# Kernel optimization log

Measured on AMD Instinct MI355X. Metric: run time of the kernel, lower is better.

## Reference

```python
import jax, jax.numpy as jnp
import numpy as np

D_MODEL, N_HEADS, D_HEAD = 1024, 16, 64
BATCH, SEQ = 4, 2048


def setup_inputs() -> dict:
    key = jax.random.key(0)
    ks = jax.random.split(key, 10)
    s = 1.0 / np.sqrt(D_MODEL)
    x = jax.random.normal(ks[0], (BATCH, SEQ, D_MODEL), dtype=jnp.float32)
    attention_mask = jax.random.randint(ks[1], (BATCH, SEQ), 0, 2).astype(jnp.bool_)
    # guarantee at least one attended key per batch row (avoid all -inf softmax)
    attention_mask = attention_mask.at[:, 0].set(True)
    def lin(k):
        kw, kb = jax.random.split(k)
        W = jax.random.uniform(kw, (D_MODEL, D_MODEL), jnp.float32, -s, s)
        b = jax.random.uniform(kb, (D_MODEL,), jnp.float32, -s, s)
        return W, b
    Wq, bq = lin(ks[2]); Wk, bk = lin(ks[3]); Wv, bv = lin(ks[4]); Wo, bo = lin(ks[5])
    return {"x": x, "attention_mask": attention_mask,
            "Wq": Wq, "bq": bq, "Wk": Wk, "bk": bk,
            "Wv": Wv, "bv": bv, "Wo": Wo, "bo": bo}


def reference(x, attention_mask, Wq, bq, Wk, bk, Wv, bv, Wo, bo):
    B, S, _ = x.shape
    def proj(W, b):  # [B,S,d_model] -> [B,S,H,Dh]
        return (x @ W + b).reshape(B, S, N_HEADS, D_HEAD)
    q = proj(Wq, bq)
    k = proj(Wk, bk)
    v = proj(Wv, bv)
    scores = jnp.einsum('bqhd,bkhd->bhqk', q, k)  # [B,H,S,S]
    add_mask = jnp.where(attention_mask, 0.0, jnp.inf)[:, None, None, :]
    # faithful order: subtract mask, THEN scale (inf survives division)
    probs = jax.nn.softmax((scores - add_mask) / jnp.sqrt(jnp.float32(D_HEAD)), axis=-1)
    attn = jnp.einsum('bhqk,bkhd->bqhd', probs, v).reshape(B, S, N_HEADS * D_HEAD)
    return attn @ Wo + bo
```

## Files before the change

kernel.cpp:

```cpp
#include <hip/hip_runtime.h>
#include <hip/hip_bf16.h>
#include <math.h>

#define BATCH 4
#define SEQ   2048
#define DM    1024
#define NH    16
#define DH    64
#define MROWS (BATCH * SEQ)

typedef unsigned short ushort_t;
typedef unsigned int   uint_t;
typedef __attribute__((ext_vector_type(8))) short  short8;
typedef __attribute__((ext_vector_type(4))) float  float4v;

#define QSCALE 0.1803368801111244f

__device__ __forceinline__ ushort_t f2bf(float v) {
    uint_t u = __float_as_uint(v);
    u += 0x7FFFu + ((u >> 16) & 1u);
    return (ushort_t)(u >> 16);
}
__device__ __forceinline__ float bf2f(ushort_t h) {
    return __uint_as_float(((uint_t)h) << 16);
}
__device__ __forceinline__ void gload_lds16(const ushort_t* g, ushort_t* lds) {
    __builtin_amdgcn_global_load_lds(
        (const __attribute__((address_space(1))) void*)g,
        (__attribute__((address_space(3))) void*)lds, 16, 0, 0);
}

__global__ __launch_bounds__(256) void conv_x(
    const float* __restrict__ src, ushort_t* __restrict__ dst, int n4)
{
    int i = blockIdx.x * 256 + threadIdx.x;
    if (i >= n4) return;
    float4 v = ((const float4*)src)[i];
    ((ushort4*)dst)[i] = make_ushort4(f2bf(v.x), f2bf(v.y), f2bf(v.z), f2bf(v.w));
}

__global__ __launch_bounds__(256) void convT_w4(
    const float* __restrict__ W0, const float* __restrict__ W1,
    const float* __restrict__ W2, const float* __restrict__ W3,
    ushort_t* __restrict__ fused, ushort_t* __restrict__ woh,
    ushort_t* __restrict__ wol)
{
    __shared__ float sT[64][65];
    const int z = blockIdx.z;
    const float* W = (z == 0) ? W0 : (z == 1) ? W1 : (z == 2) ? W2 : W3;
    ushort_t* ht = (z < 3) ? fused + (size_t)z * 1024 * 1024 : woh;
    const int n0 = blockIdx.x * 64, k0 = blockIdx.y * 64;
    const int t = threadIdx.x;
#pragma unroll
    for (int i = 0; i < 16; i++) {
        int idx = t + i * 256, r = idx >> 6, c = idx & 63;
        sT[r][c] = W[(size_t)(k0 + r) * 1024 + n0 + c];
    }
    __syncthreads();
#pragma unroll
    for (int i = 0; i < 16; i++) {
        int idx = t + i * 256, r = idx >> 6, c = idx & 63;
        float v = sT[c][r];
        ushort_t h = f2bf(v);
        ht[(size_t)(n0 + r) * 1024 + k0 + c] = h;
        if (z == 3) wol[(size_t)(n0 + r) * 1024 + k0 + c] = f2bf(v - bf2f(h));
    }
}

#define BAR()   asm volatile("s_barrier" ::: "memory")
#define LGKM0() asm volatile("s_waitcnt lgkmcnt(0)" ::: "memory")
#define VMW6()  asm volatile("s_waitcnt vmcnt(6)" ::: "memory")

#define STAGE_A(BO, KT) do {                                                 \
    const ushort_t* _s = prowA + (size_t)((KT) & 15) * 64;                   \
    gload_lds16(_s,         &smem[(BO) + dstw]);                             \
    gload_lds16(_s + 65536, &smem[(BO) + 4096 + dstw]);                      \
  } while (0)

#define STAGE_B(BO, KT) do {                                                 \
    const ushort_t* _s = prowB + (size_t)((KT) & 15) * 64;                   \
    gload_lds16(_s,          &smem[(BO) + 8192  + dstw]);                    \
    gload_lds16(_s + 65536,  &smem[(BO) + 12288 + dstw]);                    \
    gload_lds16(_s + 131072, &smem[(BO) + 16384 + dstw]);                    \
    gload_lds16(_s + 196608, &smem[(BO) + 20480 + dstw]);                    \
  } while (0)

#define LOAD_AV(BO) do {                                                     \
    _Pragma("unroll")                                                        \
    for (int mf = 0; mf < 4; mf++) {                                         \
      av[mf][0] = *(const short8*)&smem[(BO) + aAm + mf * 1024 + aA0];       \
      av[mf][1] = *(const short8*)&smem[(BO) + aAm + mf * 1024 + aA1];       \
    }                                                                        \
  } while (0)

#define LOAD_BV(BO, NQ) do {                                                 \
    _Pragma("unroll")                                                        \
    for (int nf = 0; nf < 2; nf++) {                                         \
      bvf[nf][0] = *(const short8*)&smem[(BO) + 8192 + aBn + (NQ) * 2048 +   \
                                         nf * 1024 + aA0];                   \
      bvf[nf][1] = *(const short8*)&smem[(BO) + 8192 + aBn + (NQ) * 2048 +   \
                                         nf * 1024 + aA1];                   \
    }                                                                        \
  } while (0)

#define MFMA_H(NQ) do {                                                      \
    __builtin_amdgcn_s_setprio(1);                                           \
    _Pragma("unroll")                                                        \
    for (int kk = 0; kk < 2; kk++)                                           \
      _Pragma("unroll")                                                      \
      for (int nf = 0; nf < 2; nf++)                                         \
        _Pragma("unroll")                                                    \
        for (int mf = 0; mf < 4; mf++)                                       \
          acc[mf][(NQ) * 2 + nf] =                                           \
              __builtin_amdgcn_mfma_f32_16x16x32_bf16(                       \
                  av[mf][kk], bvf[nf][kk], acc[mf][(NQ) * 2 + nf], 0, 0, 0); \
    __builtin_amdgcn_s_setprio(0);                                           \
  } while (0)

__global__ __launch_bounds__(512, 2) void gemm_qkv(
    const ushort_t* __restrict__ A, const ushort_t* __restrict__ Bt,
    const float* __restrict__ bq, const float* __restrict__ bk,
    const float* __restrict__ bv, const int* __restrict__ mask,
    ushort_t* __restrict__ Qh, ushort_t* __restrict__ Kh,
    ushort_t* __restrict__ Vt)
{
    __shared__ __align__(16) ushort_t smem[73728];
    const int t = threadIdx.x, lane = t & 63, w = t >> 6;

    int bid = blockIdx.y * 12 + blockIdx.x;
    bid = (bid & 7) * 96 + (bid >> 3);
    const int n0 = (bid % 12) * 256, m0 = (bid / 12) * 128;

    const int wm = w >> 2, wn = w & 3;
    const int lq = lane >> 4, lc = lane & 15;
    const int gl = (lane & 7) ^ ((lane >> 3) & 7);
    const int sect = n0 >> 10;
    const float* bsel = (sect == 0) ? bq : (sect == 1) ? bk : bv;
    const float scl = (sect == 0) ? QSCALE : 1.0f;

    const ushort_t* prowA = A  + (size_t)(m0 + w * 8 + (lane >> 3)) * 1024 + gl * 8;
    const ushort_t* prowB = Bt + (size_t)(n0 + w * 8 + (lane >> 3)) * 1024 + gl * 8;
    const int dstw = w * 512;

    const int aA0 = lc * 64 + ((lq ^ (lc & 7)) * 8);
    const int aA1 = lc * 64 + (((4 + lq) ^ (lc & 7)) * 8);
    const int aAm = wm * 4096;
    const int aBn = wn * 4096;

    float4v acc[4][4];
#pragma unroll
    for (int i = 0; i < 4; i++)
#pragma unroll
        for (int j = 0; j < 4; j++) acc[i][j] = (float4v)(0.0f);

    short8 av[4][2], bvf[2][2];

    STAGE_A(0, 0); STAGE_B(0, 0); STAGE_A(24576, 1); STAGE_B(24576, 1);
    VMW6();
    BAR();

    int bc = 0, bs = 49152;
    for (int kt = 0; kt < 16; kt++) {
        LOAD_AV(bc); LOAD_BV(bc, 0); STAGE_A(bs, kt + 2);
        BAR(); LGKM0(); MFMA_H(0); BAR();
        LOAD_BV(bc, 1); STAGE_B(bs, kt + 2);
        BAR(); LGKM0(); MFMA_H(1); VMW6(); BAR();
        bc = (bc == 49152) ? 0 : bc + 24576;
        bs = (bs == 49152) ? 0 : bs + 24576;
    }

#pragma unroll
    for (int nf = 0; nf < 4; nf++) {
        const int nn = (n0 + wn * 64 + nf * 16 + lc) & 1023;
        const float bvv = bsel[nn];
        const int h = nn >> 6, d = nn & 63;
#pragma unroll
        for (int mf = 0; mf < 4; mf++) {
            const int mbase = m0 + wm * 64 + mf * 16 + lq * 4;
            const int b = mbase >> 11, s0 = mbase & 2047;
            int mk[4] = {1, 1, 1, 1};
            if (sect != 0) {
                const int4 m4 = *(const int4*)&mask[b * 2048 + s0];
                mk[0] = m4.x; mk[1] = m4.y; mk[2] = m4.z; mk[3] = m4.w;
            }
            if (sect == 2) {
                ushort_t hh[4];
#pragma unroll
                for (int r = 0; r < 4; r++)
                    hh[r] = mk[r] ? f2bf(acc[mf][nf][r] + bvv) : (ushort_t)0;
                *(ushort4*)&Vt[((size_t)(b * 16 + h) * 64 + d) * 2048 + s0] =
                    make_ushort4(hh[0], hh[1], hh[2], hh[3]);
            } else {
                ushort_t* dst = (sect == 0) ? Qh : Kh;
#pragma unroll
                for (int r = 0; r < 4; r++)
                    dst[((size_t)(b * 16 + h) * 2048 + s0 + r) * 64 + d] =
                        mk[r] ? f2bf((acc[mf][nf][r] + bvv) * scl) : (ushort_t)0;
            }
        }
    }
}

#undef STAGE_A
#undef STAGE_B
#undef LOAD_AV
#undef LOAD_BV
#undef MFMA_H

#define S3_STAGE3A(BO, KT) do {                                              \
    const size_t _k = (size_t)((KT) & 31) * 32;                              \
    gload_lds16(pAh + _k, &smem[(BO) + toff]);                               \
    gload_lds16(pAl + _k, &smem[(BO) + 4096 + toff]);                        \
    gload_lds16(pBh + _k, &smem[(BO) + 8192 + toff]);                        \
  } while (0)

#define S3_STAGE3B(BO, KT) do {                                              \
    const size_t _k = (size_t)((KT) & 31) * 32;                              \
    gload_lds16(pBh + 131072 + _k, &smem[(BO) + 12288 + toff]);              \
    gload_lds16(pBl + _k,          &smem[(BO) + 16384 + toff]);              \
    gload_lds16(pBl + 131072 + _k, &smem[(BO) + 20480 + toff]);              \
  } while (0)

#define S3_MFMA(NQ) do {                                                     \
    __builtin_amdgcn_s_setprio(1);                                           \
    _Pragma("unroll")                                                        \
    for (int nf = 0; nf < 2; nf++)                                           \
      _Pragma("unroll")                                                      \
      for (int mf = 0; mf < 4; mf++) {                                       \
        float4v* _a = &acc[mf][(NQ) * 2 + nf];                               \
        *_a = __builtin_amdgcn_mfma_f32_16x16x32_bf16(ah[mf], bh[nf], *_a, 0, 0, 0); \
        *_a = __builtin_amdgcn_mfma_f32_16x16x32_bf16(al[mf], bh[nf], *_a, 0, 0, 0); \
        *_a = __builtin_amdgcn_mfma_f32_16x16x32_bf16(ah[mf], bl[nf], *_a, 0, 0, 0); \
      }                                                                      \
    __builtin_amdgcn_s_setprio(0);                                           \
  } while (0)

__global__ __launch_bounds__(512, 2) void gemm_split3(
    const ushort_t* __restrict__ Ah, const ushort_t* __restrict__ Al,
    const ushort_t* __restrict__ Bh, const ushort_t* __restrict__ Bl,
    const float* __restrict__ bias, float* __restrict__ out)
{
    __shared__ __align__(16) ushort_t smem[73728];
    const int t = threadIdx.x, lane = t & 63, w = t >> 6;

    int bid = blockIdx.y * 4 + blockIdx.x;
    bid = (bid & 7) * 32 + (bid >> 3);
    const int n0 = (bid % 4) * 256, m0 = (bid / 4) * 128;

    const int wm = w >> 2, wn = w & 3;
    const int lq = lane >> 4, lc = lane & 15;

    const int prow = t >> 2;
    const int pc = (t & 3) ^ (prow & 3);
    const size_t offA = (size_t)(m0 + prow) * 1024 + pc * 8;
    const size_t offB = (size_t)(n0 + prow) * 1024 + pc * 8;
    const ushort_t* pAh = Ah + offA;
    const ushort_t* pAl = Al + offA;
    const ushort_t* pBh = Bh + offB;
    const ushort_t* pBl = Bl + offB;
    const int toff = t * 8;

    const int aR = lc * 32 + ((lq ^ (lc & 3)) * 8);
    const int aAm = wm * 2048;
    const int aBn = wn * 2048;

    float4v acc[4][4];
#pragma unroll
    for (int i = 0; i < 4; i++)
#pragma unroll
        for (int j = 0; j < 4; j++) acc[i][j] = (float4v)(0.0f);

    short8 ah[4], al[4], bh[2], bl[2];

    S3_STAGE3A(0, 0);     S3_STAGE3B(0, 0);
    S3_STAGE3A(24576, 1); S3_STAGE3B(24576, 1);
    VMW6();
    BAR();

    int bc = 0, bs = 49152;
    for (int kt = 0; kt < 32; kt++) {
#pragma unroll
        for (int mf = 0; mf < 4; mf++) {
            ah[mf] = *(const short8*)&smem[bc + aAm + mf * 512 + aR];
            al[mf] = *(const short8*)&smem[bc + 4096 + aAm + mf * 512 + aR];
        }
#pragma unroll
        for (int nf = 0; nf < 2; nf++) {
            bh[nf] = *(const short8*)&smem[bc + 8192 + aBn + nf * 512 + aR];
            bl[nf] = *(const short8*)&smem[bc + 16384 + aBn + nf * 512 + aR];
        }
        S3_STAGE3A(bs, kt + 2);
        BAR(); LGKM0(); S3_MFMA(0); BAR();

#pragma unroll
        for (int nf = 0; nf < 2; nf++) {
            bh[nf] = *(const short8*)&smem[bc + 8192 + aBn + 1024 + nf * 512 + aR];
            bl[nf] = *(const short8*)&smem[bc + 16384 + aBn + 1024 + nf * 512 + aR];
        }
        S3_STAGE3B(bs, kt + 2);
        BAR(); LGKM0(); S3_MFMA(1); VMW6(); BAR();

        bc = (bc == 49152) ? 0 : bc + 24576;
        bs = (bs == 49152) ? 0 : bs + 24576;
    }

#pragma unroll
    for (int nf = 0; nf < 4; nf++) {
        const int n = n0 + wn * 64 + nf * 16 + lc;
        const float bvv = bias[n];
#pragma unroll
        for (int mf = 0; mf < 4; mf++)
#pragma unroll
            for (int r = 0; r < 4; r++) {
                const int m = m0 + wm * 64 + mf * 16 + lq * 4 + r;
                out[(size_t)m * 1024 + n] = acc[mf][nf][r] + bvv;
            }
    }
}

#undef S3_STAGE3A
#undef S3_STAGE3B
#undef S3_MFMA
#undef BAR
#undef LGKM0
#undef VMW6

__global__ __launch_bounds__(512, 4) void flash_mfma(
    const ushort_t* __restrict__ Q, const ushort_t* __restrict__ K,
    const ushort_t* __restrict__ Vt, const int* __restrict__ mask,
    ushort_t* __restrict__ Oh, ushort_t* __restrict__ Ol)
{
    __shared__ __align__(16) ushort_t smem[32768];
    const int t = threadIdx.x, lane = t & 63, w = t >> 6;
    const int q0 = blockIdx.x * 256;
    const int bh = blockIdx.y, b = bh >> 4, h = bh & 15;
    const int lq = lane >> 4, lc = lane & 15;
    const int wm = w * 32;
    const int gl = (lane & 7) ^ ((lane >> 3) & 7);
    const int lc7 = lc & 7;

    const short8 onesf = (short8)(lc == 0 ? (short)0x3F80 : (short)0);

    {
        const int4 a = ((const int4*)(mask + b * SEQ))[t];
        int cnt = (a.x == 0) + (a.y == 0) + (a.z == 0) + (a.w == 0);
#pragma unroll
        for (int off = 1; off < 64; off <<= 1) cnt += __shfl_xor(cnt, off);
        if (lane == 0) ((float*)&smem[28672])[w] = (float)cnt;
    }
#pragma unroll
    for (int j = 0; j < 4; j++) {
        const int i = w * 4 + j;
        gload_lds16(Q + ((size_t)bh * SEQ + q0 + i * 8 + (lane >> 3)) * 64 + gl * 8,
                    &smem[i * 512]);
    }
    const ushort_t* gsrc;
    int gstride, jstride, dstb;
    if (w < 4) {
        gsrc = K + ((size_t)bh * SEQ + w * 16 + (lane >> 3)) * 64 + gl * 8;
        gstride = 64 * 64;  jstride = 8 * 64;   dstb = 16384 + w * 1024;
    } else {
        gsrc = Vt + ((size_t)bh * 64 + (w - 4) * 16 + (lane >> 3)) * SEQ + gl * 8;
        gstride = 64;       jstride = 8 * SEQ;  dstb = 24576 + (w - 4) * 1024;
    }
    gload_lds16(gsrc,           &smem[dstb]);
    gload_lds16(gsrc + jstride, &smem[dstb + 512]);
    gsrc += gstride;

    __syncthreads();

    const float* cs = (const float*)&smem[28672];
    const float nmaskf = cs[0] + cs[1] + cs[2] + cs[3] +
                         cs[4] + cs[5] + cs[6] + cs[7];

    short8 aq[2][2];
#pragma unroll
    for (int mt = 0; mt < 2; mt++)
#pragma unroll
        for (int kk = 0; kk < 2; kk++) {
            const int r = wm + mt * 16 + lc;
            aq[mt][kk] = *(const short8*)&smem[r * 64 + (((kk * 4 + lq) ^ (r & 7)) * 8)];
        }

    int aK[2], aPw[4], aPr[2];
#pragma unroll
    for (int kk = 0; kk < 2; kk++) {
        aK[kk]  = lc * 64 + (((kk * 4 + lq) ^ lc7) * 8);
        aPr[kk] = wm * 64 + aK[kk];
    }
#pragma unroll
    for (int kt4 = 0; kt4 < 4; kt4++)
        aPw[kt4] = wm * 64 + lc * 64 + (((kt4 * 2 + (lq >> 1)) ^ lc7) * 8) + (lq & 1) * 4;

    float4v O[2][4];
    float4v lacc[2];
#pragma unroll
    for (int mt = 0; mt < 2; mt++) {
#pragma unroll
        for (int nt = 0; nt < 4; nt++) O[mt][nt] = (float4v)(0.0f);
        lacc[mt] = (float4v)(0.0f);
    }

    __syncthreads();

    for (int kt = 0; kt < 32; kt++) {
        const int cur = (kt & 1) * 4096;
        const int nxt = cur ^ 4096;

        if (kt < 31) {
            gload_lds16(gsrc,           &smem[dstb + nxt]);
            gload_lds16(gsrc + jstride, &smem[dstb + nxt + 512]);
            gsrc += gstride;
        }

#pragma unroll
        for (int kt4 = 0; kt4 < 4; kt4++) {
            float4v s0 = (float4v)(0.0f), s1 = (float4v)(0.0f);
#pragma unroll
            for (int kk = 0; kk < 2; kk++) {
                short8 ak = *(const short8*)&smem[16384 + cur + kt4 * 1024 + aK[kk]];
                s0 = __builtin_amdgcn_mfma_f32_16x16x32_bf16(ak, aq[0][kk], s0, 0, 0, 0);
                s1 = __builtin_amdgcn_mfma_f32_16x16x32_bf16(ak, aq[1][kk], s1, 0, 0, 0);
            }
            {
                const float p0 = __builtin_amdgcn_exp2f(s0[0]);
                const float p1 = __builtin_amdgcn_exp2f(s0[1]);
                const float p2 = __builtin_amdgcn_exp2f(s0[2]);
                const float p3 = __builtin_amdgcn_exp2f(s0[3]);
                __hip_bfloat162 pk01 = __float22bfloat162_rn(make_float2(p0, p1));
                __hip_bfloat162 pk23 = __float22bfloat162_rn(make_float2(p2, p3));
                *(uint2*)&smem[aPw[kt4]] =
                    make_uint2(*(const uint_t*)&pk01, *(const uint_t*)&pk23);
            }
            {
                const float p0 = __builtin_amdgcn_exp2f(s1[0]);
                const float p1 = __builtin_amdgcn_exp2f(s1[1]);
                const float p2 = __builtin_amdgcn_exp2f(s1[2]);
                const float p3 = __builtin_amdgcn_exp2f(s1[3]);
                __hip_bfloat162 pk01 = __float22bfloat162_rn(make_float2(p0, p1));
                __hip_bfloat162 pk23 = __float22bfloat162_rn(make_float2(p2, p3));
                *(uint2*)&smem[1024 + aPw[kt4]] =
                    make_uint2(*(const uint_t*)&pk01, *(const uint_t*)&pk23);
            }
        }

#pragma unroll
        for (int kk = 0; kk < 2; kk++) {
            short8 ap[2];
#pragma unroll
            for (int mt = 0; mt < 2; mt++)
                ap[mt] = *(const short8*)&smem[mt * 1024 + aPr[kk]];
            __builtin_amdgcn_s_setprio(1);
#pragma unroll
            for (int mt = 0; mt < 2; mt++)
                lacc[mt] = __builtin_amdgcn_mfma_f32_16x16x32_bf16(ap[mt], onesf, lacc[mt], 0, 0, 0);
#pragma unroll
            for (int nt = 0; nt < 4; nt++) {
                short8 bv = *(const short8*)&smem[24576 + cur + nt * 1024 + aK[kk]];
#pragma unroll
                for (int mt = 0; mt < 2; mt++)
                    O[mt][nt] = __builtin_amdgcn_mfma_f32_16x16x32_bf16(ap[mt], bv, O[mt][nt], 0, 0, 0);
            }
            __builtin_amdgcn_s_setprio(0);
        }

        asm volatile("s_waitcnt vmcnt(0)" ::: "memory");
        asm volatile("s_barrier" ::: "memory");
    }

#pragma unroll
    for (int mt = 0; mt < 2; mt++) {
#pragma unroll
        for (int r = 0; r < 4; r++) {
            const float lsum = __shfl(lacc[mt][r], lane & 48) - nmaskf;
            const float inv = 1.0f / lsum;
            const int srow = q0 + wm + mt * 16 + lq * 4 + r;
#pragma unroll
            for (int nt = 0; nt < 4; nt++) {
                const float v = O[mt][nt][r] * inv;
                const ushort_t hh = f2bf(v);
                const size_t idx = ((size_t)(b * SEQ + srow)) * 1024 + h * 64 + nt * 16 + lc;
                Oh[idx] = hh;
                Ol[idx] = f2bf(v - bf2f(hh));
            }
        }
    }
}

extern "C" void kernel_launch(void* const* d_in, const int* in_sizes, int n_in,
                              void* d_out, int out_size, void* d_ws, size_t ws_size,
                              hipStream_t stream) {
    const float* x    = (const float*)d_in[0];
    const int*   mask = (const int*)d_in[1];
    const float* Wq   = (const float*)d_in[2];
    const float* bq   = (const float*)d_in[3];
    const float* Wk   = (const float*)d_in[4];
    const float* bk   = (const float*)d_in[5];
    const float* Wv   = (const float*)d_in[6];
    const float* bv   = (const float*)d_in[7];
    const float* Wo   = (const float*)d_in[8];
    const float* bo   = (const float*)d_in[9];
    float* out = (float*)d_out;

    ushort_t* p = (ushort_t*)d_ws;
    const size_t PLANE  = (size_t)MROWS * DM;
    const size_t WPLANE = (size_t)DM * DM;
    ushort_t* xh  = p;  p += PLANE;
    ushort_t* wf  = p;  p += 3 * WPLANE;
    ushort_t* woh = p;  p += WPLANE;
    ushort_t* wol = p;  p += WPLANE;
    ushort_t* Qh  = p;  p += PLANE;
    ushort_t* Kh  = p;  p += PLANE;
    ushort_t* Vth = p;  p += PLANE;
    ushort_t* Ath = p;  p += PLANE;
    ushort_t* Atl = p;  p += PLANE;

    dim3 blk(256);
    hipLaunchKernelGGL(conv_x, dim3(8192), blk, 0, stream, x, xh, 2097152);
    hipLaunchKernelGGL(convT_w4, dim3(16, 16, 4), blk, 0, stream,
                       Wq, Wk, Wv, Wo, wf, woh, wol);
    hipLaunchKernelGGL(gemm_qkv, dim3(12, 64), dim3(512), 0, stream,
                       xh, wf, bq, bk, bv, mask, Qh, Kh, Vth);
    hipLaunchKernelGGL(flash_mfma, dim3(8, 64), dim3(512), 0, stream,
                       Qh, Kh, Vth, mask, Ath, Atl);
    hipLaunchKernelGGL(gemm_split3, dim3(4, 64), dim3(512), 0, stream,
                       Ath, Atl, woh, wol, bo, out);
}
```

Baseline: 311.4 us.

## Enlarge flash attention query tile, triple-buffer K/V, and grid-stride x conversion

The flash attention kernel now processes 512 queries per block (64 rows per wave) instead of 256. K/V tiles are shared by more MFMAs, and K/V loads go through a three-stage LDS ring with a partial vmcnt wait instead of a full drain each iteration. The row-sum is accumulated in VALU from the rounded bf16 probabilities rather than by an extra MFMA against a ones vector. The block index is remapped so neighbouring blocks share heads. The x conversion kernel becomes a 4-iteration grid-stride loop with a quarter of the blocks. Larger tiles raise register and LDS use: occupancy drops to 2 blocks per CU and the grid shrinks to 256 blocks.

```diff
diff --git a/kernel.cpp b/kernel.cpp
--- a/kernel.cpp
+++ b/kernel.cpp
@@ -34,9 +34,11 @@
     const float* __restrict__ src, ushort_t* __restrict__ dst, int n4)
 {
     int i = blockIdx.x * 256 + threadIdx.x;
-    if (i >= n4) return;
-    float4 v = ((const float4*)src)[i];
-    ((ushort4*)dst)[i] = make_ushort4(f2bf(v.x), f2bf(v.y), f2bf(v.z), f2bf(v.w));
+#pragma unroll
+    for (int k = 0; k < 4; k++, i += 524288) {
+        float4 v = ((const float4*)src)[i];
+        ((ushort4*)dst)[i] = make_ushort4(f2bf(v.x), f2bf(v.y), f2bf(v.z), f2bf(v.w));
+    }
 }
 
 __global__ __launch_bounds__(256) void convT_w4(
@@ -325,156 +327,168 @@
 #undef LGKM0
 #undef VMW6
 
-__global__ __launch_bounds__(512, 4) void flash_mfma(
+#define FBAR()  asm volatile("s_barrier" ::: "memory")
+#define FVMW4() asm volatile("s_waitcnt vmcnt(4)" ::: "memory")
+
+__global__ __launch_bounds__(512, 2) void flash_mfma(
     const ushort_t* __restrict__ Q, const ushort_t* __restrict__ K,
     const ushort_t* __restrict__ Vt, const int* __restrict__ mask,
     ushort_t* __restrict__ Oh, ushort_t* __restrict__ Ol)
 {
-    __shared__ __align__(16) ushort_t smem[32768];
+    __shared__ __align__(16) ushort_t smem[57344];
     const int t = threadIdx.x, lane = t & 63, w = t >> 6;
-    const int q0 = blockIdx.x * 256;
-    const int bh = blockIdx.y, b = bh >> 4, h = bh & 15;
-    const int lq = lane >> 4, lc = lane & 15;
-    const int wm = w * 32;
-    const int gl = (lane & 7) ^ ((lane >> 3) & 7);
-    const int lc7 = lc & 7;
-
-    const short8 onesf = (short8)(lc == 0 ? (short)0x3F80 : (short)0);
-
-    {
-        const int4 a = ((const int4*)(mask + b * SEQ))[t];
-        int cnt = (a.x == 0) + (a.y == 0) + (a.z == 0) + (a.w == 0);
-#pragma unroll
-        for (int off = 1; off < 64; off <<= 1) cnt += __shfl_xor(cnt, off);
-        if (lane == 0) ((float*)&smem[28672])[w] = (float)cnt;
-    }
-#pragma unroll
-    for (int j = 0; j < 4; j++) {
-        const int i = w * 4 + j;
-        gload_lds16(Q + ((size_t)bh * SEQ + q0 + i * 8 + (lane >> 3)) * 64 + gl * 8,
-                    &smem[i * 512]);
-    }
-    const ushort_t* gsrc;
-    int gstride, jstride, dstb;
-    if (w < 4) {
-        gsrc = K + ((size_t)bh * SEQ + w * 16 + (lane >> 3)) * 64 + gl * 8;
-        gstride = 64 * 64;  jstride = 8 * 64;   dstb = 16384 + w * 1024;
-    } else {
-        gsrc = Vt + ((size_t)bh * 64 + (w - 4) * 16 + (lane >> 3)) * SEQ + gl * 8;
-        gstride = 64;       jstride = 8 * SEQ;  dstb = 24576 + (w - 4) * 1024;
-    }
-    gload_lds16(gsrc,           &smem[dstb]);
-    gload_lds16(gsrc + jstride, &smem[dstb + 512]);
-    gsrc += gstride;
-
-    __syncthreads();
-
-    const float* cs = (const float*)&smem[28672];
+
+    const int i = blockIdx.y * 4 + blockIdx.x;
+    const int bh = (i & 7) + ((i >> 5) << 3);
+    const int q0 = ((i >> 3) & 3) * 512;
+    const int b = bh >> 4, h = bh & 15;
+
+    const int lq = lane >> 4, lc = lane & 15, lc7 = lc & 7;
+    const int wq = w * 64;
+
+    const int4 ma = ((const int4*)(mask + b * SEQ))[t];
+
+    const int trow = lane >> 3;
+    const int gl = (lane & 7) ^ (trow & 7);
+    const ushort_t* qsrc = Q + ((size_t)bh * SEQ + q0 + wq + trow) * 64 + gl * 8;
+#pragma unroll
+    for (int j = 0; j < 8; j++)
+        gload_lds16(qsrc + j * 512, &smem[w * 4096 + j * 512 + lane * 8]);
+
+    const int strow = t >> 3;
+    const int sgl = (t & 7) ^ (strow & 7);
+    const ushort_t* kbase = K  + ((size_t)bh * SEQ + strow) * 64 + sgl * 8;
+    const ushort_t* vbase = Vt + ((size_t)bh * 64 + strow) * SEQ + sgl * 8;
+    gload_lds16(kbase,        &smem[32768 + t * 8]);
+    gload_lds16(vbase,        &smem[45056 + t * 8]);
+    gload_lds16(kbase + 4096, &smem[32768 + 4096 + t * 8]);
+    gload_lds16(vbase + 64,   &smem[45056 + 4096 + t * 8]);
+
+    int cnt = (ma.x == 0) + (ma.y == 0) + (ma.z == 0) + (ma.w == 0);
+#pragma unroll
+    for (int off = 1; off < 64; off <<= 1) cnt += __shfl_xor(cnt, off);
+    if (lane == 0) ((float*)&smem[40960])[w] = (float)cnt;
+
+    FBAR();
+
+    const float* cs = (const float*)&smem[40960];
     const float nmaskf = cs[0] + cs[1] + cs[2] + cs[3] +
                          cs[4] + cs[5] + cs[6] + cs[7];
 
-    short8 aq[2][2];
-#pragma unroll
-    for (int mt = 0; mt < 2; mt++)
+    FVMW4();
+    short8 aq[4][2];
+#pragma unroll
+    for (int mt = 0; mt < 4; mt++)
 #pragma unroll
         for (int kk = 0; kk < 2; kk++) {
-            const int r = wm + mt * 16 + lc;
-            aq[mt][kk] = *(const short8*)&smem[r * 64 + (((kk * 4 + lq) ^ (r & 7)) * 8)];
-        }
-
-    int aK[2], aPw[4], aPr[2];
-#pragma unroll
-    for (int kk = 0; kk < 2; kk++) {
-        aK[kk]  = lc * 64 + (((kk * 4 + lq) ^ lc7) * 8);
-        aPr[kk] = wm * 64 + aK[kk];
-    }
+            const int r = mt * 16 + lc;
+            aq[mt][kk] = *(const short8*)&smem[w * 4096 + r * 64 +
+                                               (((kk * 4 + lq) ^ (r & 7)) * 8)];
+        }
+    FBAR();
+
+    int aK[2], aPw[4];
+#pragma unroll
+    for (int kk = 0; kk < 2; kk++)
+        aK[kk] = lc * 64 + (((kk * 4 + lq) ^ lc7) * 8);
 #pragma unroll
     for (int kt4 = 0; kt4 < 4; kt4++)
-        aPw[kt4] = wm * 64 + lc * 64 + (((kt4 * 2 + (lq >> 1)) ^ lc7) * 8) + (lq & 1) * 4;
-
-    float4v O[2][4];
-    float4v lacc[2];
-#pragma unroll
-    for (int mt = 0; mt < 2; mt++) {
+        aPw[kt4] = lc * 64 + (((kt4 * 2 + (lq >> 1)) ^ lc7) * 8) + (lq & 1) * 4;
+
+    float4v O[4][4];
+    float ladd[4];
+#pragma unroll
+    for (int mt = 0; mt < 4; mt++) {
 #pragma unroll
         for (int nt = 0; nt < 4; nt++) O[mt][nt] = (float4v)(0.0f);
-        lacc[mt] = (float4v)(0.0f);
-    }
-
-    __syncthreads();
-
+        ladd[mt] = 0.0f;
+    }
+
+    int cb = 0, sb = 2;
     for (int kt = 0; kt < 32; kt++) {
-        const int cur = (kt & 1) * 4096;
-        const int nxt = cur ^ 4096;
-
-        if (kt < 31) {
-            gload_lds16(gsrc,           &smem[dstb + nxt]);
-            gload_lds16(gsrc + jstride, &smem[dstb + nxt + 512]);
-            gsrc += gstride;
-        }
+        const int kn = (kt + 2) & 31;
+        gload_lds16(kbase + kn * 4096, &smem[32768 + sb * 4096 + t * 8]);
+        gload_lds16(vbase + kn * 64,   &smem[45056 + sb * 4096 + t * 8]);
+        FVMW4();
+        FBAR();
+
+        const int kb = 32768 + cb * 4096;
+        const int vb = 45056 + cb * 4096;
+        const int pb = w * 4096;
 
 #pragma unroll
         for (int kt4 = 0; kt4 < 4; kt4++) {
-            float4v s0 = (float4v)(0.0f), s1 = (float4v)(0.0f);
+            float4v sc[4];
+#pragma unroll
+            for (int mt = 0; mt < 4; mt++) sc[mt] = (float4v)(0.0f);
 #pragma unroll
             for (int kk = 0; kk < 2; kk++) {
-                short8 ak = *(const short8*)&smem[16384 + cur + kt4 * 1024 + aK[kk]];
-                s0 = __builtin_amdgcn_mfma_f32_16x16x32_bf16(ak, aq[0][kk], s0, 0, 0, 0);
-                s1 = __builtin_amdgcn_mfma_f32_16x16x32_bf16(ak, aq[1][kk], s1, 0, 0, 0);
-            }
-            {
-                const float p0 = __builtin_amdgcn_exp2f(s0[0]);
-                const float p1 = __builtin_amdgcn_exp2f(s0[1]);
-                const float p2 = __builtin_amdgcn_exp2f(s0[2]);
-                const float p3 = __builtin_amdgcn_exp2f(s0[3]);
+                const short8 ak = *(const short8*)&smem[kb + kt4 * 1024 + aK[kk]];
+#pragma unroll
+                for (int mt = 0; mt < 4; mt++)
+                    sc[mt] = __builtin_amdgcn_mfma_f32_16x16x32_bf16(ak, aq[mt][kk], sc[mt], 0, 0, 0);
+            }
+#pragma unroll
+            for (int mt = 0; mt < 4; mt++) {
+                const float p0 = __builtin_amdgcn_exp2f(sc[mt][0]);
+                const float p1 = __builtin_amdgcn_exp2f(sc[mt][1]);
+                const float p2 = __builtin_amdgcn_exp2f(sc[mt][2]);
+                const float p3 = __builtin_amdgcn_exp2f(sc[mt][3]);
                 __hip_bfloat162 pk01 = __float22bfloat162_rn(make_float2(p0, p1));
                 __hip_bfloat162 pk23 = __float22bfloat162_rn(make_float2(p2, p3));
-                *(uint2*)&smem[aPw[kt4]] =
-                    make_uint2(*(const uint_t*)&pk01, *(const uint_t*)&pk23);
-            }
-            {
-                const float p0 = __builtin_amdgcn_exp2f(s1[0]);
-                const float p1 = __builtin_amdgcn_exp2f(s1[1]);
-                const float p2 = __builtin_amdgcn_exp2f(s1[2]);
-                const float p3 = __builtin_amdgcn_exp2f(s1[3]);
-                __hip_bfloat162 pk01 = __float22bfloat162_rn(make_float2(p0, p1));
-                __hip_bfloat162 pk23 = __float22bfloat162_rn(make_float2(p2, p3));
-                *(uint2*)&smem[1024 + aPw[kt4]] =
-                    make_uint2(*(const uint_t*)&pk01, *(const uint_t*)&pk23);
+                const uint_t u01 = *(const uint_t*)&pk01;
+                const uint_t u23 = *(const uint_t*)&pk23;
+                ladd[mt] += __uint_as_float(u01 << 16) + __uint_as_float(u01 & 0xffff0000u)
+                          + __uint_as_float(u23 << 16) + __uint_as_float(u23 & 0xffff0000u);
+                *(uint2*)&smem[pb + mt * 1024 + aPw[kt4]] = make_uint2(u01, u23);
             }
         }
 
 #pragma unroll
         for (int kk = 0; kk < 2; kk++) {
-            short8 ap[2];
-#pragma unroll
-            for (int mt = 0; mt < 2; mt++)
-                ap[mt] = *(const short8*)&smem[mt * 1024 + aPr[kk]];
+            short8 ap[4];
+#pragma unroll
+            for (int mt = 0; mt < 4; mt++)
+                ap[mt] = *(const short8*)&smem[pb + mt * 1024 + aK[kk]];
             __builtin_amdgcn_s_setprio(1);
 #pragma unroll
-            for (int mt = 0; mt < 2; mt++)
-                lacc[mt] = __builtin_amdgcn_mfma_f32_16x16x32_bf16(ap[mt], onesf, lacc[mt], 0, 0, 0);
-#pragma unroll
             for (int nt = 0; nt < 4; nt++) {
-                short8 bv = *(const short8*)&smem[24576 + cur + nt * 1024 + aK[kk]];
-#pragma unroll
-                for (int mt = 0; mt < 2; mt++)
+                const short8 bv = *(const short8*)&smem[vb + nt * 1024 + aK[kk]];
+#pragma unroll
+                for (int mt = 0; mt < 4; mt++)
                     O[mt][nt] = __builtin_amdgcn_mfma_f32_16x16x32_bf16(ap[mt], bv, O[mt][nt], 0, 0, 0);
             }
             __builtin_amdgcn_s_setprio(0);
         }
-
-        asm volatile("s_waitcnt vmcnt(0)" ::: "memory");
-        asm volatile("s_barrier" ::: "memory");
-    }
-
-#pragma unroll
-    for (int mt = 0; mt < 2; mt++) {
+        FBAR();
+
+        cb = (cb == 2) ? 0 : cb + 1;
+        sb = (sb == 2) ? 0 : sb + 1;
+    }
+
+    float lred[4];
+#pragma unroll
+    for (int mt = 0; mt < 4; mt++) {
+        float v = ladd[mt];
+        v += __shfl_xor(v, 16);
+        v += __shfl_xor(v, 32);
+        lred[mt] = v;
+    }
+    if (lq == 0) {
+#pragma unroll
+        for (int mt = 0; mt < 4; mt++)
+            ((float*)smem)[w * 2048 + mt * 16 + lc] = lred[mt];
+    }
+    __syncthreads();
+
+#pragma unroll
+    for (int mt = 0; mt < 4; mt++) {
 #pragma unroll
         for (int r = 0; r < 4; r++) {
-            const float lsum = __shfl(lacc[mt][r], lane & 48) - nmaskf;
+            const float lsum =
+                ((const float*)smem)[w * 2048 + mt * 16 + lq * 4 + r] - nmaskf;
             const float inv = 1.0f / lsum;
-            const int srow = q0 + wm + mt * 16 + lq * 4 + r;
+            const int srow = q0 + wq + mt * 16 + lq * 4 + r;
 #pragma unroll
             for (int nt = 0; nt < 4; nt++) {
                 const float v = O[mt][nt][r] * inv;
@@ -486,6 +500,9 @@
         }
     }
 }
+
+#undef FBAR
+#undef FVMW4
 
 extern "C" void kernel_launch(void* const* d_in, const int* in_sizes, int n_in,
                               void* d_out, int out_size, void* d_ws, size_t ws_size,
@@ -516,12 +533,12 @@
     ushort_t* Atl = p;  p += PLANE;
 
     dim3 blk(256);
-    hipLaunchKernelGGL(conv_x, dim3(8192), blk, 0, stream, x, xh, 2097152);
+    hipLaunchKernelGGL(conv_x, dim3(2048), blk, 0, stream, x, xh, 2097152);
     hipLaunchKernelGGL(convT_w4, dim3(16, 16, 4), blk, 0, stream,
                        Wq, Wk, Wv, Wo, wf, woh, wol);
     hipLaunchKernelGGL(gemm_qkv, dim3(12, 64), dim3(512), 0, stream,
                        xh, wf, bq, bk, bv, mask, Qh, Kh, Vth);
-    hipLaunchKernelGGL(flash_mfma, dim3(8, 64), dim3(512), 0, stream,
+    hipLaunchKernelGGL(flash_mfma, dim3(4, 64), dim3(512), 0, stream,
                        Qh, Kh, Vth, mask, Ath, Atl);
     hipLaunchKernelGGL(gemm_split3, dim3(4, 64), dim3(512), 0, stream,
                        Ath, Atl, woh, wol, bo, out);
```

Result: slower. 323.8 us (+4.0%).

## Merge conversion kernels into one launch and remap flash attention block order

Applied to the files above, without the earlier changes.

Combines the x bf16 conversion and the weight transpose/convert kernels into a single prep launch: the first 2048 blocks each convert four float4s per thread, and the remaining 1024 blocks transpose the weights. This removes one kernel launch and its inter-kernel gap. It also remaps the flash attention grid so that consecutive blocks cover different batch-head pairs and the query tile varies slowest, which changes how work is spread across CUs and how K/V is reused in cache. The remap risks worse L2 locality if K/V sharing between query tiles of the same head was helping.

```diff
diff --git a/kernel.cpp b/kernel.cpp
--- a/kernel.cpp
+++ b/kernel.cpp
@@ -30,27 +30,31 @@
         (__attribute__((address_space(3))) void*)lds, 16, 0, 0);
 }
 
-__global__ __launch_bounds__(256) void conv_x(
-    const float* __restrict__ src, ushort_t* __restrict__ dst, int n4)
-{
-    int i = blockIdx.x * 256 + threadIdx.x;
-    if (i >= n4) return;
-    float4 v = ((const float4*)src)[i];
-    ((ushort4*)dst)[i] = make_ushort4(f2bf(v.x), f2bf(v.y), f2bf(v.z), f2bf(v.w));
-}
-
-__global__ __launch_bounds__(256) void convT_w4(
+__global__ __launch_bounds__(256) void prep(
+    const float* __restrict__ x, ushort_t* __restrict__ xh,
     const float* __restrict__ W0, const float* __restrict__ W1,
     const float* __restrict__ W2, const float* __restrict__ W3,
     ushort_t* __restrict__ fused, ushort_t* __restrict__ woh,
     ushort_t* __restrict__ wol)
 {
     __shared__ float sT[64][65];
-    const int z = blockIdx.z;
+    const int t = threadIdx.x;
+
+    if (blockIdx.x < 2048) {
+        int i = blockIdx.x * 256 + t;
+#pragma unroll
+        for (int k = 0; k < 4; k++, i += 524288) {
+            float4 v = ((const float4*)x)[i];
+            ((ushort4*)xh)[i] = make_ushort4(f2bf(v.x), f2bf(v.y), f2bf(v.z), f2bf(v.w));
+        }
+        return;
+    }
+
+    const int id = blockIdx.x - 2048;
+    const int z = id >> 8;
     const float* W = (z == 0) ? W0 : (z == 1) ? W1 : (z == 2) ? W2 : W3;
     ushort_t* ht = (z < 3) ? fused + (size_t)z * 1024 * 1024 : woh;
-    const int n0 = blockIdx.x * 64, k0 = blockIdx.y * 64;
-    const int t = threadIdx.x;
+    const int n0 = (id & 15) * 64, k0 = ((id >> 4) & 15) * 64;
 #pragma unroll
     for (int i = 0; i < 16; i++) {
         int idx = t + i * 256, r = idx >> 6, c = idx & 63;
@@ -332,8 +336,12 @@
 {
     __shared__ __align__(16) ushort_t smem[32768];
     const int t = threadIdx.x, lane = t & 63, w = t >> 6;
-    const int q0 = blockIdx.x * 256;
-    const int bh = blockIdx.y, b = bh >> 4, h = bh & 15;
+
+    const int i = blockIdx.x + blockIdx.y * 8;
+    const int bh = (i & 7) + 8 * ((i >> 3) & 7);
+    const int q0 = (i >> 6) * 256;
+    const int b = bh >> 4, h = bh & 15;
+
     const int lq = lane >> 4, lc = lane & 15;
     const int wm = w * 32;
     const int gl = (lane & 7) ^ ((lane >> 3) & 7);
@@ -350,9 +358,9 @@
     }
 #pragma unroll
     for (int j = 0; j < 4; j++) {
-        const int i = w * 4 + j;
-        gload_lds16(Q + ((size_t)bh * SEQ + q0 + i * 8 + (lane >> 3)) * 64 + gl * 8,
-                    &smem[i * 512]);
+        const int i2 = w * 4 + j;
+        gload_lds16(Q + ((size_t)bh * SEQ + q0 + i2 * 8 + (lane >> 3)) * 64 + gl * 8,
+                    &smem[i2 * 512]);
     }
     const ushort_t* gsrc;
     int gstride, jstride, dstb;
@@ -516,9 +524,8 @@
     ushort_t* Atl = p;  p += PLANE;
 
     dim3 blk(256);
-    hipLaunchKernelGGL(conv_x, dim3(8192), blk, 0, stream, x, xh, 2097152);
-    hipLaunchKernelGGL(convT_w4, dim3(16, 16, 4), blk, 0, stream,
-                       Wq, Wk, Wv, Wo, wf, woh, wol);
+    hipLaunchKernelGGL(prep, dim3(3072), blk, 0, stream,
+                       x, xh, Wq, Wk, Wv, Wo, wf, woh, wol);
     hipLaunchKernelGGL(gemm_qkv, dim3(12, 64), dim3(512), 0, stream,
                        xh, wf, bq, bk, bv, mask, Qh, Kh, Vth);
     hipLaunchKernelGGL(flash_mfma, dim3(8, 64), dim3(512), 0, stream,
```

Measured after the change: 309.2 us. No clear change (-0.7%).
